# Performance work log

Hardware: AMD Instinct MI355X
Metric: run time of the kernel (lower is better)

The kernel has to match this reference:

```python
import jax, jax.numpy as jnp
import numpy as np


def setup_inputs() -> dict:
    key = jax.random.key(0)
    k1, k2, k3, k4 = jax.random.split(key, 4)
    B, S, D_IN, D_OUT = 4, 2048, 4096, 16384
    x = jax.random.normal(k1, (B, S, D_IN), dtype=jnp.float32)
    # compressed (int8-style) weight, stored [in_features, out_features] per Conv1D convention
    w_q = jax.random.randint(k2, (D_IN, D_OUT), -127, 127, dtype=jnp.int32)
    # per-output-channel dequant scale
    scale = jax.random.uniform(k3, (D_OUT,), dtype=jnp.float32) * 0.01 + 1e-4
    bias = jax.random.normal(k4, (D_OUT,), dtype=jnp.float32)
    return {"x": x, "w_q": w_q, "scale": scale, "bias": bias}


def reference(x, w_q, scale, bias):
    # Dequantize compressed weight: W[i, o] = w_q[i, o] * scale[o]
    w = w_q.astype(jnp.float32) * scale[None, :]  # [D_in, D_out]
    # Conv1D forward: y = x @ W + b
    y = jnp.einsum('bsi,io->bso', x, w) + bias
    return y
```

## Files before the change

### kernel.cpp

```cpp
#include <hip/hip_runtime.h>


#define M_DIM 8192
#define K_DIM 4096
#define N_DIM 16384

#define BM 256
#define BN 256
#define BK 64
#define NT (K_DIM / BK)
#define NWG ((M_DIM / BM) * (N_DIM / BN))

typedef unsigned short u16;
typedef __attribute__((ext_vector_type(8))) short short8;
typedef __attribute__((ext_vector_type(4))) float floatx4;

__device__ __forceinline__ u16 f2bf(float f) {
    unsigned int u = __builtin_bit_cast(unsigned int, f);
    u += 0x7fffu + ((u >> 16) & 1u);
    return (u16)(u >> 16);
}

__global__ __launch_bounds__(256) void cvt_x_kernel(const float4* __restrict__ x,
                                                    uint4* __restrict__ out) {
    int i = blockIdx.x * 256 + threadIdx.x;
    float4 a = x[2 * i];
    float4 b = x[2 * i + 1];
    uint4 o;
    o.x = (unsigned)f2bf(a.x) | ((unsigned)f2bf(a.y) << 16);
    o.y = (unsigned)f2bf(a.z) | ((unsigned)f2bf(a.w) << 16);
    o.z = (unsigned)f2bf(b.x) | ((unsigned)f2bf(b.y) << 16);
    o.w = (unsigned)f2bf(b.z) | ((unsigned)f2bf(b.w) << 16);
    out[i] = o;
}

__global__ __launch_bounds__(256) void transpose_wq(const int* __restrict__ wq,
                                                    u16* __restrict__ wT) {
    __shared__ u16 tile[64][65];
    const int n0 = blockIdx.x * 64;
    const int k0 = blockIdx.y * 64;
    const int tx = threadIdx.x;
    const int ty = threadIdx.y;
    #pragma unroll
    for (int r = 0; r < 4; ++r) {
        int kl = ty + 16 * r;
        const int4 v = *(const int4*)(wq + (size_t)(k0 + kl) * N_DIM + n0 + tx * 4);
        tile[kl][tx * 4 + 0] = f2bf((float)v.x);
        tile[kl][tx * 4 + 1] = f2bf((float)v.y);
        tile[kl][tx * 4 + 2] = f2bf((float)v.z);
        tile[kl][tx * 4 + 3] = f2bf((float)v.w);
    }
    __syncthreads();
    #pragma unroll
    for (int r = 0; r < 4; ++r) {
        int nl = ty + 16 * r;
        ushort4 o;
        o.x = tile[tx * 4 + 0][nl];
        o.y = tile[tx * 4 + 1][nl];
        o.z = tile[tx * 4 + 2][nl];
        o.w = tile[tx * 4 + 3][nl];
        *(ushort4*)(wT + (size_t)(n0 + nl) * K_DIM + k0 + tx * 4) = o;
    }
}

__device__ __forceinline__ void async_copy16(const u16* gptr, u16* ldsptr) {
    __builtin_amdgcn_global_load_lds(
        (const __attribute__((address_space(1))) void*)gptr,
        (__attribute__((address_space(3))) void*)ldsptr,
        16, 0, 0);
}

__global__ __launch_bounds__(512, 2) void gemm_bf16(const u16* __restrict__ A,
                                                    const u16* __restrict__ Bt,
                                                    const float* __restrict__ scale,
                                                    const float* __restrict__ bias,
                                                    float* __restrict__ C) {
    __shared__ u16 smem[65536];

    const int tid  = threadIdx.x;
    const int lane = tid & 63;
    const int wave = tid >> 6;
    const int wr   = wave >> 2;
    const int wc   = wave & 3;
    const int fr   = lane & 15;
    const int quad = lane >> 4;

    int wg = blockIdx.x;
    wg = (wg & 7) * (NWG / 8) + (wg >> 3);
    const int grp = wg >> 9;
    const int rem = wg & 511;
    const int by  = grp * 8 + (rem & 7);
    const int bx  = rem >> 3;
    const int m0 = by * BM;
    const int n0 = bx * BN;

    const int sw   = fr & 7;
    const int sl0  = (quad ^ sw) * 8;
    const int sl1  = sl0 ^ 32;
    const int rA   = fr * 64;
    const int aBase0 = wr * 8192;
    const int bBase0 = 16384 + (wc >> 1) * 8192 + (wc & 1) * 4096;

    const int srow  = tid >> 3;
    const int sslot = ((tid & 7) ^ (srow & 7)) * 8;
    const int ldst  = tid * 8;

#define STAGE_A(t_, h_, p_) do {                                               \
    const u16* g_ = A + (size_t)(m0 + (h_) * 128 + srow) * K_DIM + (t_) * BK + sslot; \
    u16* l_ = smem + (p_) * 32768 + (h_) * 8192 + ldst;                        \
    async_copy16(g_, l_);                                                      \
    async_copy16(g_ + (size_t)64 * K_DIM, l_ + 4096);                          \
} while (0)

#define STAGE_B(t_, h_, p_) do {                                               \
    const u16* g_ = Bt + (size_t)(n0 + (h_) * 128 + srow) * K_DIM + (t_) * BK + sslot; \
    u16* l_ = smem + (p_) * 32768 + 16384 + (h_) * 8192 + ldst;                \
    async_copy16(g_, l_);                                                      \
    async_copy16(g_ + (size_t)64 * K_DIM, l_ + 4096);                          \
} while (0)

    floatx4 acc[8][4];
    #pragma unroll
    for (int i = 0; i < 8; ++i)
        #pragma unroll
        for (int j = 0; j < 4; ++j)
            acc[i][j] = (floatx4){0.f, 0.f, 0.f, 0.f};

    STAGE_A(0, 0, 0); STAGE_A(0, 1, 0); STAGE_B(0, 0, 0); STAGE_B(0, 1, 0);
    STAGE_A(1, 0, 1); STAGE_A(1, 1, 1); STAGE_B(1, 0, 1); STAGE_B(1, 1, 1);
    asm volatile("s_waitcnt vmcnt(8)" ::: "memory");
    __builtin_amdgcn_s_barrier();
    __builtin_amdgcn_sched_barrier(0);

    short8 af[4][2], bfv[4][2];

    for (int t = 0; t < NT; ++t) {
        const int p = t & 1;
        const u16* SA = smem + p * 32768 + aBase0;
        const u16* SB = smem + p * 32768 + bBase0;

        #pragma unroll
        for (int i = 0; i < 4; ++i) {
            af[i][0] = *(const short8*)(SA + i * 1024 + rA + sl0);
            af[i][1] = *(const short8*)(SA + i * 1024 + rA + sl1);
        }
        #pragma unroll
        for (int j = 0; j < 2; ++j) {
            bfv[j][0] = *(const short8*)(SB + j * 1024 + rA + sl0);
            bfv[j][1] = *(const short8*)(SB + j * 1024 + rA + sl1);
        }
        __builtin_amdgcn_s_barrier();
        asm volatile("s_waitcnt lgkmcnt(0)" ::: "memory");
        __builtin_amdgcn_s_setprio(1);
        #pragma unroll
        for (int i = 0; i < 4; ++i)
            #pragma unroll
            for (int j = 0; j < 2; ++j) {
                acc[i][j] = __builtin_amdgcn_mfma_f32_16x16x32_bf16(af[i][0], bfv[j][0], acc[i][j], 0, 0, 0);
                acc[i][j] = __builtin_amdgcn_mfma_f32_16x16x32_bf16(af[i][1], bfv[j][1], acc[i][j], 0, 0, 0);
            }
        __builtin_amdgcn_s_setprio(0);
        __builtin_amdgcn_s_barrier();
        __builtin_amdgcn_sched_barrier(0);

        #pragma unroll
        for (int j = 2; j < 4; ++j) {
            bfv[j][0] = *(const short8*)(SB + j * 1024 + rA + sl0);
            bfv[j][1] = *(const short8*)(SB + j * 1024 + rA + sl1);
        }
        __builtin_amdgcn_s_barrier();
        asm volatile("s_waitcnt lgkmcnt(0)" ::: "memory");
        __builtin_amdgcn_s_setprio(1);
        #pragma unroll
        for (int i = 0; i < 4; ++i)
            #pragma unroll
            for (int j = 2; j < 4; ++j) {
                acc[i][j] = __builtin_amdgcn_mfma_f32_16x16x32_bf16(af[i][0], bfv[j][0], acc[i][j], 0, 0, 0);
                acc[i][j] = __builtin_amdgcn_mfma_f32_16x16x32_bf16(af[i][1], bfv[j][1], acc[i][j], 0, 0, 0);
            }
        __builtin_amdgcn_s_setprio(0);
        __builtin_amdgcn_s_barrier();
        __builtin_amdgcn_sched_barrier(0);

        #pragma unroll
        for (int i = 0; i < 4; ++i) {
            af[i][0] = *(const short8*)(SA + (i + 4) * 1024 + rA + sl0);
            af[i][1] = *(const short8*)(SA + (i + 4) * 1024 + rA + sl1);
        }
        if (t < NT - 2) { STAGE_B(t + 2, 0, p); STAGE_B(t + 2, 1, p); }
        __builtin_amdgcn_s_barrier();
        asm volatile("s_waitcnt lgkmcnt(0)" ::: "memory");
        __builtin_amdgcn_s_setprio(1);
        #pragma unroll
        for (int i = 0; i < 4; ++i)
            #pragma unroll
            for (int j = 0; j < 2; ++j) {
                acc[i + 4][j] = __builtin_amdgcn_mfma_f32_16x16x32_bf16(af[i][0], bfv[j][0], acc[i + 4][j], 0, 0, 0);
                acc[i + 4][j] = __builtin_amdgcn_mfma_f32_16x16x32_bf16(af[i][1], bfv[j][1], acc[i + 4][j], 0, 0, 0);
            }
        __builtin_amdgcn_s_setprio(0);
        __builtin_amdgcn_s_barrier();
        __builtin_amdgcn_sched_barrier(0);

        if (t < NT - 2) { STAGE_A(t + 2, 0, p); STAGE_A(t + 2, 1, p); }
        __builtin_amdgcn_s_barrier();
        __builtin_amdgcn_s_setprio(1);
        #pragma unroll
        for (int i = 0; i < 4; ++i)
            #pragma unroll
            for (int j = 2; j < 4; ++j) {
                acc[i + 4][j] = __builtin_amdgcn_mfma_f32_16x16x32_bf16(af[i][0], bfv[j][0], acc[i + 4][j], 0, 0, 0);
                acc[i + 4][j] = __builtin_amdgcn_mfma_f32_16x16x32_bf16(af[i][1], bfv[j][1], acc[i + 4][j], 0, 0, 0);
            }
        __builtin_amdgcn_s_setprio(0);
        if (t < NT - 2) {
            asm volatile("s_waitcnt vmcnt(8)" ::: "memory");
        } else if (t == NT - 2) {
            asm volatile("s_waitcnt vmcnt(0)" ::: "memory");
        }
        __builtin_amdgcn_s_barrier();
        __builtin_amdgcn_sched_barrier(0);
    }

    #pragma unroll
    for (int j = 0; j < 4; ++j) {
        const int col = n0 + wc * 64 + j * 16 + fr;
        const float s = scale[col];
        const float b = bias[col];
        #pragma unroll
        for (int i = 0; i < 8; ++i) {
            const int rowb = m0 + wr * 128 + i * 16 + quad * 4;
            #pragma unroll
            for (int r = 0; r < 4; ++r)
                C[(size_t)(rowb + r) * N_DIM + col] = acc[i][j][r] * s + b;
        }
    }
#undef STAGE_A
#undef STAGE_B
}

extern "C" void kernel_launch(void* const* d_in, const int* in_sizes, int n_in,
                              void* d_out, int out_size, void* d_ws, size_t ws_size,
                              hipStream_t stream) {
    const float* x     = (const float*)d_in[0];
    const int*   wq    = (const int*)d_in[1];
    const float* scale = (const float*)d_in[2];
    const float* bias  = (const float*)d_in[3];
    float* y = (float*)d_out;

    u16* wT = (u16*)d_ws;
    u16* xb = (u16*)((char*)d_ws + (size_t)N_DIM * K_DIM * 2);

    cvt_x_kernel<<<(M_DIM * (size_t)K_DIM) / (256 * 8), 256, 0, stream>>>(
        (const float4*)x, (uint4*)xb);
    transpose_wq<<<dim3(N_DIM / 64, K_DIM / 64), dim3(16, 16), 0, stream>>>(wq, wT);
    gemm_bf16<<<dim3(NWG), 512, 0, stream>>>(xb, wT, scale, bias, y);
}
```

Measured before the change: 1.756 ms.

## Split K-tile into halves and prefetch A one stage ahead

The main loop now works through each BK tile in two K-halves (sl0, then sl1). Each phase loads a single short8 fragment per A and B sub-tile, which halves the fragment register arrays. The A tile for the next step is staged into the other LDS buffer early in the iteration, replacing the previous distance-2 A prefetch, while B keeps distance-2 prefetching; the vmcnt waits are adjusted to match. The aim is to lower VGPR pressure and rebalance global-to-LDS traffic against MFMA work. The cost is a shorter A prefetch distance, which may expose more global latency.

```diff
diff --git a/kernel.cpp b/kernel.cpp
--- a/kernel.cpp
+++ b/kernel.cpp
@@ -127,94 +127,86 @@
             acc[i][j] = (floatx4){0.f, 0.f, 0.f, 0.f};
 
     STAGE_A(0, 0, 0); STAGE_A(0, 1, 0); STAGE_B(0, 0, 0); STAGE_B(0, 1, 0);
-    STAGE_A(1, 0, 1); STAGE_A(1, 1, 1); STAGE_B(1, 0, 1); STAGE_B(1, 1, 1);
-    asm volatile("s_waitcnt vmcnt(8)" ::: "memory");
+    STAGE_B(1, 0, 1); STAGE_B(1, 1, 1);
+    asm volatile("s_waitcnt vmcnt(4)" ::: "memory");
     __builtin_amdgcn_s_barrier();
     __builtin_amdgcn_sched_barrier(0);
 
-    short8 af[4][2], bfv[4][2];
+    short8 af[4], bfv[4];
 
     for (int t = 0; t < NT; ++t) {
-        const int p = t & 1;
+        const int p  = t & 1;
+        const int pn = p ^ 1;
         const u16* SA = smem + p * 32768 + aBase0;
         const u16* SB = smem + p * 32768 + bBase0;
 
         #pragma unroll
-        for (int i = 0; i < 4; ++i) {
-            af[i][0] = *(const short8*)(SA + i * 1024 + rA + sl0);
-            af[i][1] = *(const short8*)(SA + i * 1024 + rA + sl1);
-        }
-        #pragma unroll
-        for (int j = 0; j < 2; ++j) {
-            bfv[j][0] = *(const short8*)(SB + j * 1024 + rA + sl0);
-            bfv[j][1] = *(const short8*)(SB + j * 1024 + rA + sl1);
-        }
-        __builtin_amdgcn_s_barrier();
-        asm volatile("s_waitcnt lgkmcnt(0)" ::: "memory");
-        __builtin_amdgcn_s_setprio(1);
-        #pragma unroll
-        for (int i = 0; i < 4; ++i)
-            #pragma unroll
-            for (int j = 0; j < 2; ++j) {
-                acc[i][j] = __builtin_amdgcn_mfma_f32_16x16x32_bf16(af[i][0], bfv[j][0], acc[i][j], 0, 0, 0);
-                acc[i][j] = __builtin_amdgcn_mfma_f32_16x16x32_bf16(af[i][1], bfv[j][1], acc[i][j], 0, 0, 0);
-            }
-        __builtin_amdgcn_s_setprio(0);
-        __builtin_amdgcn_s_barrier();
-        __builtin_amdgcn_sched_barrier(0);
-
-        #pragma unroll
-        for (int j = 2; j < 4; ++j) {
-            bfv[j][0] = *(const short8*)(SB + j * 1024 + rA + sl0);
-            bfv[j][1] = *(const short8*)(SB + j * 1024 + rA + sl1);
-        }
-        __builtin_amdgcn_s_barrier();
-        asm volatile("s_waitcnt lgkmcnt(0)" ::: "memory");
-        __builtin_amdgcn_s_setprio(1);
-        #pragma unroll
-        for (int i = 0; i < 4; ++i)
-            #pragma unroll
-            for (int j = 2; j < 4; ++j) {
-                acc[i][j] = __builtin_amdgcn_mfma_f32_16x16x32_bf16(af[i][0], bfv[j][0], acc[i][j], 0, 0, 0);
-                acc[i][j] = __builtin_amdgcn_mfma_f32_16x16x32_bf16(af[i][1], bfv[j][1], acc[i][j], 0, 0, 0);
-            }
-        __builtin_amdgcn_s_setprio(0);
-        __builtin_amdgcn_s_barrier();
-        __builtin_amdgcn_sched_barrier(0);
-
-        #pragma unroll
-        for (int i = 0; i < 4; ++i) {
-            af[i][0] = *(const short8*)(SA + (i + 4) * 1024 + rA + sl0);
-            af[i][1] = *(const short8*)(SA + (i + 4) * 1024 + rA + sl1);
-        }
-        if (t < NT - 2) { STAGE_B(t + 2, 0, p); STAGE_B(t + 2, 1, p); }
-        __builtin_amdgcn_s_barrier();
-        asm volatile("s_waitcnt lgkmcnt(0)" ::: "memory");
-        __builtin_amdgcn_s_setprio(1);
-        #pragma unroll
-        for (int i = 0; i < 4; ++i)
-            #pragma unroll
-            for (int j = 0; j < 2; ++j) {
-                acc[i + 4][j] = __builtin_amdgcn_mfma_f32_16x16x32_bf16(af[i][0], bfv[j][0], acc[i + 4][j], 0, 0, 0);
-                acc[i + 4][j] = __builtin_amdgcn_mfma_f32_16x16x32_bf16(af[i][1], bfv[j][1], acc[i + 4][j], 0, 0, 0);
-            }
-        __builtin_amdgcn_s_setprio(0);
-        __builtin_amdgcn_s_barrier();
-        __builtin_amdgcn_sched_barrier(0);
-
-        if (t < NT - 2) { STAGE_A(t + 2, 0, p); STAGE_A(t + 2, 1, p); }
-        __builtin_amdgcn_s_barrier();
-        __builtin_amdgcn_s_setprio(1);
-        #pragma unroll
-        for (int i = 0; i < 4; ++i)
-            #pragma unroll
-            for (int j = 2; j < 4; ++j) {
-                acc[i + 4][j] = __builtin_amdgcn_mfma_f32_16x16x32_bf16(af[i][0], bfv[j][0], acc[i + 4][j], 0, 0, 0);
-                acc[i + 4][j] = __builtin_amdgcn_mfma_f32_16x16x32_bf16(af[i][1], bfv[j][1], acc[i + 4][j], 0, 0, 0);
-            }
+        for (int i = 0; i < 4; ++i)
+            af[i] = *(const short8*)(SA + i * 1024 + rA + sl0);
+        #pragma unroll
+        for (int j = 0; j < 4; ++j)
+            bfv[j] = *(const short8*)(SB + j * 1024 + rA + sl0);
+        if (t + 1 < NT) { STAGE_A(t + 1, 0, pn); STAGE_A(t + 1, 1, pn); }
+        __builtin_amdgcn_s_barrier();
+        asm volatile("s_waitcnt lgkmcnt(0)" ::: "memory");
+        __builtin_amdgcn_s_setprio(1);
+        #pragma unroll
+        for (int i = 0; i < 4; ++i)
+            #pragma unroll
+            for (int j = 0; j < 4; ++j)
+                acc[i][j] = __builtin_amdgcn_mfma_f32_16x16x32_bf16(af[i], bfv[j], acc[i][j], 0, 0, 0);
+        __builtin_amdgcn_s_setprio(0);
+        __builtin_amdgcn_s_barrier();
+        __builtin_amdgcn_sched_barrier(0);
+
+        #pragma unroll
+        for (int i = 0; i < 4; ++i)
+            af[i] = *(const short8*)(SA + (i + 4) * 1024 + rA + sl0);
+        __builtin_amdgcn_s_barrier();
+        asm volatile("s_waitcnt lgkmcnt(0)" ::: "memory");
+        __builtin_amdgcn_s_setprio(1);
+        #pragma unroll
+        for (int i = 0; i < 4; ++i)
+            #pragma unroll
+            for (int j = 0; j < 4; ++j)
+                acc[i + 4][j] = __builtin_amdgcn_mfma_f32_16x16x32_bf16(af[i], bfv[j], acc[i + 4][j], 0, 0, 0);
+        __builtin_amdgcn_s_setprio(0);
+        __builtin_amdgcn_s_barrier();
+        __builtin_amdgcn_sched_barrier(0);
+
+        #pragma unroll
+        for (int i = 0; i < 4; ++i)
+            af[i] = *(const short8*)(SA + i * 1024 + rA + sl1);
+        #pragma unroll
+        for (int j = 0; j < 4; ++j)
+            bfv[j] = *(const short8*)(SB + j * 1024 + rA + sl1);
+        __builtin_amdgcn_s_barrier();
+        asm volatile("s_waitcnt lgkmcnt(0)" ::: "memory");
+        __builtin_amdgcn_s_setprio(1);
+        #pragma unroll
+        for (int i = 0; i < 4; ++i)
+            #pragma unroll
+            for (int j = 0; j < 4; ++j)
+                acc[i][j] = __builtin_amdgcn_mfma_f32_16x16x32_bf16(af[i], bfv[j], acc[i][j], 0, 0, 0);
+        __builtin_amdgcn_s_setprio(0);
+        __builtin_amdgcn_s_barrier();
+        __builtin_amdgcn_sched_barrier(0);
+
+        #pragma unroll
+        for (int i = 0; i < 4; ++i)
+            af[i] = *(const short8*)(SA + (i + 4) * 1024 + rA + sl1);
+        if (t + 2 < NT) { STAGE_B(t + 2, 0, p); STAGE_B(t + 2, 1, p); }
+        __builtin_amdgcn_s_barrier();
+        asm volatile("s_waitcnt lgkmcnt(0)" ::: "memory");
+        __builtin_amdgcn_s_setprio(1);
+        #pragma unroll
+        for (int i = 0; i < 4; ++i)
+            #pragma unroll
+            for (int j = 0; j < 4; ++j)
+                acc[i + 4][j] = __builtin_amdgcn_mfma_f32_16x16x32_bf16(af[i], bfv[j], acc[i + 4][j], 0, 0, 0);
         __builtin_amdgcn_s_setprio(0);
         if (t < NT - 2) {
-            asm volatile("s_waitcnt vmcnt(8)" ::: "memory");
+            asm volatile("s_waitcnt vmcnt(4)" ::: "memory");
         } else if (t == NT - 2) {
             asm volatile("s_waitcnt vmcnt(0)" ::: "memory");
         }
```

New measurement: 1.715 ms. 2.3% less time.
